# Performance work log

Hardware: AMD Instinct MI355X
Metric: run time of the kernel (lower is better)

The kernel has to match this reference:

```python
import jax, jax.numpy as jnp
import numpy as np

B, T, D = 8, 1024, 128
TEMP = 0.1
WEIGHT = 1.0


def _neg_scaled_l2(x, y):
    # x: [P, T, D], y: [P, S, D] -> -||x-y||^2 / D / TEMP  (l2 similarity, normalize_dimension=True)
    x2 = jnp.sum(x * x, axis=-1)[..., :, None]            # [P, T, 1]
    y2 = jnp.sum(y * y, axis=-1)[..., None, :]            # [P, 1, S]
    xy = jnp.einsum('ptd,psd->pts', x, y)                 # [P, T, S]
    d2 = jnp.maximum(x2 + y2 - 2.0 * xy, 0.0)             # cdist(...)**2 is non-negative
    return -d2 / D / TEMP


def setup_inputs() -> dict:
    key = jax.random.key(0)
    k1, k2, k3 = jax.random.split(key, 3)
    embs = jax.random.normal(k1, (B, T, D), dtype=jnp.float32)
    frame_idxs = jnp.sort(jax.random.randint(k2, (B, T), 0, 4096, dtype=jnp.int32), axis=-1)
    video_len = jax.random.randint(k3, (B,), T, 4096, dtype=jnp.int32)
    return {"embs": embs, "frame_idxs": frame_idxs, "video_len": video_len}


def reference(embs, frame_idxs, video_len):
    # All ordered pairs (i, j) with i != j, built at trace time.
    pairs = np.array([(i, j) for i in range(B) for j in range(B) if i != j])
    ii, jj = pairs[:, 0], pairs[:, 1]                     # [P]

    e1 = embs[ii]                                         # [P, T, D]
    e2 = embs[jj]                                         # [P, T, D]

    # Cycle: soft nearest neighbors of e1 in e2, then align back to e1.
    sim12 = _neg_scaled_l2(e1, e2)                        # [P, T, T]
    beta12 = jax.nn.softmax(sim12, axis=-1)
    nn_embs = jnp.einsum('pts,psd->ptd', beta12, e2)      # [P, T, D]
    logits = _neg_scaled_l2(nn_embs, e1)                  # [P, T, T]

    beta = jax.nn.softmax(logits, axis=-1)                # [P, T, T]
    steps = frame_idxs.astype(jnp.float32) / video_len.astype(jnp.float32)[:, None]  # [B, T]
    sp = steps[ii]                                        # [P, T] (steps of sequence i)
    time_true = sp                                        # one_hot(labels) picks the diagonal
    time_pred = jnp.einsum('pts,ps->pt', beta, sp)        # [P, T]
    loss = jnp.mean((time_pred - time_true) ** 2)
    return WEIGHT * loss
```

## Files before the change

### kernel.cpp

```cpp
#include <hip/hip_runtime.h>
#include <hip/hip_bf16.h>


#define T_ 1024
#define D_ 128
#define NPAIR 56
#define NSCALE 0.11271055006945026f
#define SQDS 0.474785316f

typedef float f32x16 __attribute__((ext_vector_type(16)));

#define B8F 131072
#define B8T 163840

__device__ __forceinline__ unsigned short f2bf(float f) {
  unsigned u = __float_as_uint(f);
  u += 0x7fff + ((u >> 16) & 1);
  return (unsigned short)(u >> 16);
}
__device__ __forceinline__ float bf2f(unsigned short v) {
  return __uint_as_float(((unsigned)v) << 16);
}
__device__ __forceinline__ float clamp8(float x) {
  return fminf(fmaxf(x, -440.f), 440.f);
}
__device__ __forceinline__ unsigned pk4(float a, float b, float c, float d) {
  int w = __builtin_amdgcn_cvt_pk_fp8_f32(a, b, 0, false);
  w = __builtin_amdgcn_cvt_pk_fp8_f32(c, d, w, true);
  return (unsigned)w;
}
__device__ __forceinline__ float waveSum(float v) {
#pragma unroll
  for (int k = 32; k >= 1; k >>= 1) v += __shfl_xor(v, k, 64);
  return v;
}
__device__ __forceinline__ void stage1k(const unsigned char* g, unsigned char* lds, int lane) {
  __builtin_amdgcn_global_load_lds(
      (const __attribute__((address_space(1))) unsigned int*)(g + lane * 16),
      (__attribute__((address_space(3))) unsigned int*)lds, 16, 0, 0);
}

__device__ __forceinline__ void c2b8(const unsigned* m, int lh, long long* b0, long long* b1) {
  unsigned send0 = lh ? m[0] : m[1];
  unsigned send1 = lh ? m[2] : m[3];
  unsigned r0 = (unsigned)__shfl_xor((int)send0, 32, 64);
  unsigned r1 = (unsigned)__shfl_xor((int)send1, 32, 64);
  union { unsigned u[2]; long long ll; } x0, x1;
  x0.u[0] = lh ? r0 : m[0];  x0.u[1] = lh ? m[1] : r0;
  x1.u[0] = lh ? r1 : m[2];  x1.u[1] = lh ? m[3] : r1;
  *b0 = x0.ll; *b1 = x1.ll;
}

#define MFMA8(A, B, C) __builtin_amdgcn_mfma_f32_32x32x16_fp8_fp8((A), (B), (C), 0, 0, 0)
#define LD8(P, Q) (*(const long long*)((P) + (Q) * 512))
#define EXPC(x) fminf(__builtin_amdgcn_exp2f(x), 448.f)
#define WAITV(N) asm volatile("s_waitcnt vmcnt(" #N ")" ::: "memory")
#define BAR() do { asm volatile("" ::: "memory"); __builtin_amdgcn_s_barrier(); asm volatile("" ::: "memory"); } while (0)

__global__ __launch_bounds__(256) void convert_kernel(
    const float* __restrict__ embs, const int* __restrict__ fi,
    const int* __restrict__ vl, unsigned char* __restrict__ e8F,
    unsigned char* __restrict__ e8T, float* __restrict__ steps,
    float* __restrict__ acc, unsigned* __restrict__ cnt) {
  __shared__ unsigned short tileS[32 * 136];
  __shared__ float psum[32][8];
  __shared__ float g_sh[32], sp_sh[32];
  const int b = blockIdx.x >> 5;
  const int t0 = (blockIdx.x & 31) * 32;
  const int tid = threadIdx.x;
  const int row = tid >> 3, seg = tid & 7;

  if (blockIdx.x == 0 && tid == 0) { acc[0] = 0.f; cnt[0] = 0u; }

  const float* src = embs + (size_t)(b * T_ + t0 + row) * D_ + seg * 16;
  float4 g4[4];
#pragma unroll
  for (int k = 0; k < 4; k++) g4[k] = ((const float4*)src)[k];
  float s = 0.f;
  float fv[16];
#pragma unroll
  for (int k = 0; k < 4; k++) {
    s += g4[k].x * g4[k].x + g4[k].y * g4[k].y + g4[k].z * g4[k].z + g4[k].w * g4[k].w;
    fv[4 * k + 0] = g4[k].x * SQDS; fv[4 * k + 1] = g4[k].y * SQDS;
    fv[4 * k + 2] = g4[k].z * SQDS; fv[4 * k + 3] = g4[k].w * SQDS;
  }
  psum[row][seg] = s;

  {
    unsigned char* dstA = e8F + (size_t)b * B8F + (size_t)((t0 >> 5) * 8 + seg) * 512;
    uint2 lo, hi;
    lo.x = pk4(fv[0], fv[1], fv[2], fv[3]);   lo.y = pk4(fv[4], fv[5], fv[6], fv[7]);
    hi.x = pk4(fv[8], fv[9], fv[10], fv[11]); hi.y = pk4(fv[12], fv[13], fv[14], fv[15]);
    *(uint2*)(dstA + row * 8) = lo;
    *(uint2*)(dstA + (size_t)(32 + row) * 8) = hi;
  }
#pragma unroll
  for (int k = 0; k < 16; k++) tileS[row * 136 + seg * 16 + k] = f2bf(fv[k]);
  __syncthreads();

  if (tid < 32) {
    float t = 0.f;
#pragma unroll
    for (int k = 0; k < 8; k++) t += psum[tid][k];
    int gr = b * T_ + t0 + tid;
    float sp = (float)fi[gr] / (float)vl[b];
    steps[gr] = sp;
    sp_sh[tid] = sp;
    g_sh[tid] = __builtin_amdgcn_exp2f(14.0f - t * NSCALE);
  }
  __syncthreads();

  {
    const int c8 = tid >> 5;
    const int n2 = c8 & 3, scp = c8 >> 2;
    const int dd = n2 * 32 + (tid & 31);
#pragma unroll
    for (int half = 0; half < 2; half++) {
      const int lane = half * 32 + (tid & 31);
      const int sl = scp * 16 + half * 8;
      float vv[8];
#pragma unroll
      for (int jj = 0; jj < 8; jj++)
        vv[jj] = clamp8(bf2f(tileS[(sl + jj) * 136 + dd]) * g_sh[sl + jj]);
      uint2 wv;
      wv.x = pk4(vv[0], vv[1], vv[2], vv[3]);
      wv.y = pk4(vv[4], vv[5], vv[6], vv[7]);
      int c = n2 * 64 + (t0 >> 4) + scp;
      *(uint2*)(e8T + (size_t)b * B8T + (size_t)c * 512 + lane * 8) = wv;
    }
  }
  if (tid < 128) {
    const int sc2 = tid >> 6, lane = tid & 63;
    const int m = lane & 31, kh = lane >> 5;
    uint2 wv; wv.x = 0u; wv.y = 0u;
    if (m < 2) {
      float vv[8];
#pragma unroll
      for (int e = 0; e < 8; e++) {
        int sl = sc2 * 16 + kh * 8 + e;
        float gg = g_sh[sl];
        vv[e] = clamp8(m ? gg * sp_sh[sl] : gg);
      }
      wv.x = pk4(vv[0], vv[1], vv[2], vv[3]);
      wv.y = pk4(vv[4], vv[5], vv[6], vv[7]);
    }
    int c = 256 + (t0 >> 4) + sc2;
    *(uint2*)(e8T + (size_t)b * B8T + (size_t)c * 512 + lane * 8) = wv;
  }
}

__global__ __launch_bounds__(256, 2) void tcc_main(
    const unsigned char* __restrict__ e8F, const unsigned char* __restrict__ e8T,
    const float* __restrict__ steps, float* __restrict__ loss_acc,
    unsigned* __restrict__ cnt, float* __restrict__ out) {
  __shared__ unsigned char smem[55296];
  __shared__ float blred[4];
  unsigned char* kt = smem;
  unsigned char* vt = smem + 24576;
  unsigned char* gt = smem + 24576;

  const int bx = blockIdx.x;
  const int pair = bx >> 3;
  const int tile = bx & 7;
  const int i = pair / 7;
  const int r = pair % 7;
  const int j = r + (r >= i ? 1 : 0);
  const int tid = threadIdx.x;
  const int w = tid >> 6;
  const int l = tid & 63;
  const int l31 = l & 31;
  const int lh = l >> 5;
  const int tb = tile * 128 + w * 32;

  const unsigned char* eFi = e8F + (size_t)i * B8F;
  const unsigned char* eFj = e8F + (size_t)j * B8F;
  const unsigned char* eTj = e8T + (size_t)j * B8T;
  const unsigned char* eTi = e8T + (size_t)i * B8T;

  long long qf8[8];
  {
    const unsigned char* qb = eFi + (size_t)((tb >> 5) * 8) * 512 + l * 8;
#pragma unroll
    for (int kc = 0; kc < 8; kc++) qf8[kc] = LD8(qb, kc);
  }

  const f32x16 Z = {0.f, 0.f, 0.f, 0.f, 0.f, 0.f, 0.f, 0.f,
                    0.f, 0.f, 0.f, 0.f, 0.f, 0.f, 0.f, 0.f};
  const f32x16 CM6 = {-6.f, -6.f, -6.f, -6.f, -6.f, -6.f, -6.f, -6.f,
                      -6.f, -6.f, -6.f, -6.f, -6.f, -6.f, -6.f, -6.f};
  f32x16 o[5];
#pragma unroll
  for (int n2 = 0; n2 < 5; n2++) o[n2] = Z;

  auto stageP1 = [&](int t, int b) {
    stage1k(eFj + (size_t)(8 * t + 2 * w) * 1024, kt + b * 8192 + (2 * w) * 1024, l);
    stage1k(eFj + (size_t)(8 * t + 2 * w + 1) * 1024, kt + b * 8192 + (2 * w + 1) * 1024, l);
#pragma unroll
    for (int u = 0; u < 3; u++) {
      int vu = w + 4 * u;
      if (vu < 10) {
        int n2v = vu >> 1, uh = vu & 1;
        stage1k(eTj + (size_t)(n2v * 32 + t * 2 + uh) * 1024, vt + b * 10240 + vu * 1024, l);
      }
    }
  };
  auto stageP2 = [&](int t, int b) {
    stage1k(eFi + (size_t)(8 * t + 2 * w) * 1024, kt + b * 8192 + (2 * w) * 1024, l);
    stage1k(eFi + (size_t)(8 * t + 2 * w + 1) * 1024, kt + b * 8192 + (2 * w + 1) * 1024, l);
    if (w < 2) stage1k(eTi + (size_t)(128 + t * 2 + w) * 1024, gt + b * 2048 + w * 1024, l);
  };

  stageP1(0, 0);
  stageP1(1, 1);
  WAITV(0);
  BAR();

  f32x16 ca0, ca1;
  {
    const unsigned char* kb = kt + l * 8;
    ca0 = MFMA8(LD8(kb, 0), qf8[0], CM6);
    ca1 = MFMA8(LD8(kb, 8), qf8[0], CM6);
#pragma unroll
    for (int dc = 1; dc < 8; dc++) {
      ca0 = MFMA8(LD8(kb, dc), qf8[dc], ca0);
      ca1 = MFMA8(LD8(kb, 8 + dc), qf8[dc], ca1);
    }
  }

  {
    int cur = 0, nxt = 1, pre = 2;
    for (int st = 0; st < 16; st++) {
      if (st <= 13) stageP1(st + 2, pre);
      __builtin_amdgcn_sched_barrier(0);

      f32x16 cb0, cb1;
      if (st < 15) {
        const unsigned char* kb = kt + nxt * 8192 + l * 8;
        cb0 = MFMA8(LD8(kb, 0), qf8[0], CM6);
        cb1 = MFMA8(LD8(kb, 8), qf8[0], CM6);
#pragma unroll
        for (int dc = 1; dc < 8; dc++) {
          cb0 = MFMA8(LD8(kb, dc), qf8[dc], cb0);
          cb1 = MFMA8(LD8(kb, 8 + dc), qf8[dc], cb1);
        }
      }

      unsigned m0[4], m1[4];
#pragma unroll
      for (int k2 = 0; k2 < 4; k2++) {
        m0[k2] = pk4(EXPC(ca0[4 * k2]), EXPC(ca0[4 * k2 + 1]),
                     EXPC(ca0[4 * k2 + 2]), EXPC(ca0[4 * k2 + 3]));
        m1[k2] = pk4(EXPC(ca1[4 * k2]), EXPC(ca1[4 * k2 + 1]),
                     EXPC(ca1[4 * k2 + 2]), EXPC(ca1[4 * k2 + 3]));
      }
      long long pB[4];
      c2b8(m0, lh, &pB[0], &pB[1]);
      c2b8(m1, lh, &pB[2], &pB[3]);

      const unsigned char* vb = vt + cur * 10240 + l * 8;
#pragma unroll
      for (int n2 = 0; n2 < 5; n2++)
#pragma unroll
        for (int sc = 0; sc < 4; sc++)
          o[n2] = MFMA8(LD8(vb, n2 * 4 + sc), pB[sc], o[n2]);

      if (st <= 13) {
        WAITV(0);
        BAR();
      } else if (st == 15) {
        BAR();
      }
      if (st < 15) { ca0 = cb0; ca1 = cb1; }
      int tswap = cur; cur = nxt; nxt = pre; pre = tswap;
    }
  }

  stageP2(0, 0);
  stageP2(1, 1);

  float Lme = o[4][0];
  float Lo = __shfl_xor(Lme, 32, 64);
  float inv = 1.0f / (lh ? Lo : Lme);
  long long qf2[8];
#pragma unroll
  for (int n2 = 0; n2 < 4; n2++) {
    unsigned mm[4];
#pragma unroll
    for (int k2 = 0; k2 < 4; k2++)
      mm[k2] = pk4(o[n2][4 * k2] * inv, o[n2][4 * k2 + 1] * inv,
                   o[n2][4 * k2 + 2] * inv, o[n2][4 * k2 + 3] * inv);
    c2b8(mm, lh, &qf2[2 * n2], &qf2[2 * n2 + 1]);
  }
  f32x16 acc6 = Z;
  WAITV(0);
  BAR();

  f32x16 da0, da1;
  {
    const unsigned char* kb = kt + l * 8;
    da0 = MFMA8(LD8(kb, 0), qf2[0], CM6);
    da1 = MFMA8(LD8(kb, 8), qf2[0], CM6);
#pragma unroll
    for (int dc = 1; dc < 8; dc++) {
      da0 = MFMA8(LD8(kb, dc), qf2[dc], da0);
      da1 = MFMA8(LD8(kb, 8 + dc), qf2[dc], da1);
    }
  }

  {
    int cur = 0, nxt = 1, pre = 2;
    for (int st = 0; st < 16; st++) {
      if (st <= 13) stageP2(st + 2, pre);
      __builtin_amdgcn_sched_barrier(0);

      f32x16 db0, db1;
      if (st < 15) {
        const unsigned char* kb = kt + nxt * 8192 + l * 8;
        db0 = MFMA8(LD8(kb, 0), qf2[0], CM6);
        db1 = MFMA8(LD8(kb, 8), qf2[0], CM6);
#pragma unroll
        for (int dc = 1; dc < 8; dc++) {
          db0 = MFMA8(LD8(kb, dc), qf2[dc], db0);
          db1 = MFMA8(LD8(kb, 8 + dc), qf2[dc], db1);
        }
      }

      unsigned m0[4], m1[4];
#pragma unroll
      for (int k2 = 0; k2 < 4; k2++) {
        m0[k2] = pk4(EXPC(da0[4 * k2]), EXPC(da0[4 * k2 + 1]),
                     EXPC(da0[4 * k2 + 2]), EXPC(da0[4 * k2 + 3]));
        m1[k2] = pk4(EXPC(da1[4 * k2]), EXPC(da1[4 * k2 + 1]),
                     EXPC(da1[4 * k2 + 2]), EXPC(da1[4 * k2 + 3]));
      }
      long long pB[4];
      c2b8(m0, lh, &pB[0], &pB[1]);
      c2b8(m1, lh, &pB[2], &pB[3]);

      const unsigned char* gb = gt + cur * 2048 + l * 8;
#pragma unroll
      for (int sc = 0; sc < 4; sc++)
        acc6 = MFMA8(LD8(gb, sc), pB[sc], acc6);

      if (st <= 13) {
        WAITV(0);
        BAR();
      }
      if (st < 15) { da0 = db0; da1 = db1; }
      int tswap = cur; cur = nxt; nxt = pre; pre = tswap;
    }
  }

  float local = 0.f;
  if (lh == 0) {
    float pred = acc6[1] / acc6[0];
    float tt = steps[i * T_ + tb + l31];
    float dd = pred - tt;
    local = dd * dd;
  }
  local = waveSum(local);
  if (l == 0) blred[w] = local;
  __syncthreads();
  if (tid == 0) {
    atomicAdd(loss_acc, blred[0] + blred[1] + blred[2] + blred[3]);
    __threadfence();
    unsigned old = atomicAdd(cnt, 1u);
    if (old == (unsigned)(gridDim.x - 1)) {
      float v = atomicAdd(loss_acc, 0.0f);
      out[0] = v * (1.0f / (float)(NPAIR * T_));
    }
  }
}

extern "C" void kernel_launch(void* const* d_in, const int* in_sizes, int n_in,
                              void* d_out, int out_size, void* d_ws, size_t ws_size,
                              hipStream_t stream) {
  const float* embs = (const float*)d_in[0];
  const int* frame_idxs = (const int*)d_in[1];
  const int* video_len = (const int*)d_in[2];
  float* out = (float*)d_out;

  char* ws = (char*)d_ws;
  float* acc = (float*)ws;
  unsigned* cnt = (unsigned*)(ws + 512);
  float* steps = (float*)(ws + 4096);
  unsigned char* e8F = (unsigned char*)(ws + 65536);
  unsigned char* e8T = e8F + (size_t)8 * B8F;

  convert_kernel<<<dim3(256), dim3(256), 0, stream>>>(embs, frame_idxs, video_len,
                                                      e8F, e8T, steps, acc, cnt);
  tcc_main<<<dim3(NPAIR * 8), dim3(256), 0, stream>>>(e8F, e8T, steps, acc, cnt, out);
}
```

Measured before the change: 114.4 us.

## Fuse conversion kernel into main kernel with a global spin-wait barrier

```diff
diff --git a/kernel.cpp b/kernel.cpp
--- a/kernel.cpp
+++ b/kernel.cpp
@@ -57,102 +57,12 @@
 #define WAITV(N) asm volatile("s_waitcnt vmcnt(" #N ")" ::: "memory")
 #define BAR() do { asm volatile("" ::: "memory"); __builtin_amdgcn_s_barrier(); asm volatile("" ::: "memory"); } while (0)
 
-__global__ __launch_bounds__(256) void convert_kernel(
+__global__ __launch_bounds__(256, 2) void fused_main(
     const float* __restrict__ embs, const int* __restrict__ fi,
     const int* __restrict__ vl, unsigned char* __restrict__ e8F,
     unsigned char* __restrict__ e8T, float* __restrict__ steps,
-    float* __restrict__ acc, unsigned* __restrict__ cnt) {
-  __shared__ unsigned short tileS[32 * 136];
-  __shared__ float psum[32][8];
-  __shared__ float g_sh[32], sp_sh[32];
-  const int b = blockIdx.x >> 5;
-  const int t0 = (blockIdx.x & 31) * 32;
-  const int tid = threadIdx.x;
-  const int row = tid >> 3, seg = tid & 7;
-
-  if (blockIdx.x == 0 && tid == 0) { acc[0] = 0.f; cnt[0] = 0u; }
-
-  const float* src = embs + (size_t)(b * T_ + t0 + row) * D_ + seg * 16;
-  float4 g4[4];
-#pragma unroll
-  for (int k = 0; k < 4; k++) g4[k] = ((const float4*)src)[k];
-  float s = 0.f;
-  float fv[16];
-#pragma unroll
-  for (int k = 0; k < 4; k++) {
-    s += g4[k].x * g4[k].x + g4[k].y * g4[k].y + g4[k].z * g4[k].z + g4[k].w * g4[k].w;
-    fv[4 * k + 0] = g4[k].x * SQDS; fv[4 * k + 1] = g4[k].y * SQDS;
-    fv[4 * k + 2] = g4[k].z * SQDS; fv[4 * k + 3] = g4[k].w * SQDS;
-  }
-  psum[row][seg] = s;
-
-  {
-    unsigned char* dstA = e8F + (size_t)b * B8F + (size_t)((t0 >> 5) * 8 + seg) * 512;
-    uint2 lo, hi;
-    lo.x = pk4(fv[0], fv[1], fv[2], fv[3]);   lo.y = pk4(fv[4], fv[5], fv[6], fv[7]);
-    hi.x = pk4(fv[8], fv[9], fv[10], fv[11]); hi.y = pk4(fv[12], fv[13], fv[14], fv[15]);
-    *(uint2*)(dstA + row * 8) = lo;
-    *(uint2*)(dstA + (size_t)(32 + row) * 8) = hi;
-  }
-#pragma unroll
-  for (int k = 0; k < 16; k++) tileS[row * 136 + seg * 16 + k] = f2bf(fv[k]);
-  __syncthreads();
-
-  if (tid < 32) {
-    float t = 0.f;
-#pragma unroll
-    for (int k = 0; k < 8; k++) t += psum[tid][k];
-    int gr = b * T_ + t0 + tid;
-    float sp = (float)fi[gr] / (float)vl[b];
-    steps[gr] = sp;
-    sp_sh[tid] = sp;
-    g_sh[tid] = __builtin_amdgcn_exp2f(14.0f - t * NSCALE);
-  }
-  __syncthreads();
-
-  {
-    const int c8 = tid >> 5;
-    const int n2 = c8 & 3, scp = c8 >> 2;
-    const int dd = n2 * 32 + (tid & 31);
-#pragma unroll
-    for (int half = 0; half < 2; half++) {
-      const int lane = half * 32 + (tid & 31);
-      const int sl = scp * 16 + half * 8;
-      float vv[8];
-#pragma unroll
-      for (int jj = 0; jj < 8; jj++)
-        vv[jj] = clamp8(bf2f(tileS[(sl + jj) * 136 + dd]) * g_sh[sl + jj]);
-      uint2 wv;
-      wv.x = pk4(vv[0], vv[1], vv[2], vv[3]);
-      wv.y = pk4(vv[4], vv[5], vv[6], vv[7]);
-      int c = n2 * 64 + (t0 >> 4) + scp;
-      *(uint2*)(e8T + (size_t)b * B8T + (size_t)c * 512 + lane * 8) = wv;
-    }
-  }
-  if (tid < 128) {
-    const int sc2 = tid >> 6, lane = tid & 63;
-    const int m = lane & 31, kh = lane >> 5;
-    uint2 wv; wv.x = 0u; wv.y = 0u;
-    if (m < 2) {
-      float vv[8];
-#pragma unroll
-      for (int e = 0; e < 8; e++) {
-        int sl = sc2 * 16 + kh * 8 + e;
-        float gg = g_sh[sl];
-        vv[e] = clamp8(m ? gg * sp_sh[sl] : gg);
-      }
-      wv.x = pk4(vv[0], vv[1], vv[2], vv[3]);
-      wv.y = pk4(vv[4], vv[5], vv[6], vv[7]);
-    }
-    int c = 256 + (t0 >> 4) + sc2;
-    *(uint2*)(e8T + (size_t)b * B8T + (size_t)c * 512 + lane * 8) = wv;
-  }
-}
-
-__global__ __launch_bounds__(256, 2) void tcc_main(
-    const unsigned char* __restrict__ e8F, const unsigned char* __restrict__ e8T,
-    const float* __restrict__ steps, float* __restrict__ loss_acc,
-    unsigned* __restrict__ cnt, float* __restrict__ out) {
+    float* __restrict__ loss_acc, unsigned* __restrict__ cnt,
+    unsigned* __restrict__ cvt, float* __restrict__ out) {
   __shared__ unsigned char smem[55296];
   __shared__ float blred[4];
   unsigned char* kt = smem;
@@ -160,12 +70,108 @@
   unsigned char* gt = smem + 24576;
 
   const int bx = blockIdx.x;
+  const int tid = threadIdx.x;
+
+  if (bx < 256) {
+    unsigned short* tileS = (unsigned short*)smem;
+    float* psum = (float*)(smem + 8704);
+    float* g_sh = (float*)(smem + 9728);
+    float* sp_sh = (float*)(smem + 9856);
+    const int b = bx >> 5;
+    const int t0 = (bx & 31) * 32;
+    const int row = tid >> 3, seg = tid & 7;
+
+    const float* src = embs + (size_t)(b * T_ + t0 + row) * D_ + seg * 16;
+    float4 g4[4];
+#pragma unroll
+    for (int k = 0; k < 4; k++) g4[k] = ((const float4*)src)[k];
+    float s = 0.f;
+    float fv[16];
+#pragma unroll
+    for (int k = 0; k < 4; k++) {
+      s += g4[k].x * g4[k].x + g4[k].y * g4[k].y + g4[k].z * g4[k].z + g4[k].w * g4[k].w;
+      fv[4 * k + 0] = g4[k].x * SQDS; fv[4 * k + 1] = g4[k].y * SQDS;
+      fv[4 * k + 2] = g4[k].z * SQDS; fv[4 * k + 3] = g4[k].w * SQDS;
+    }
+    psum[row * 8 + seg] = s;
+
+    {
+      unsigned char* dstA = e8F + (size_t)b * B8F + (size_t)((t0 >> 5) * 8 + seg) * 512;
+      uint2 lo, hi;
+      lo.x = pk4(fv[0], fv[1], fv[2], fv[3]);   lo.y = pk4(fv[4], fv[5], fv[6], fv[7]);
+      hi.x = pk4(fv[8], fv[9], fv[10], fv[11]); hi.y = pk4(fv[12], fv[13], fv[14], fv[15]);
+      *(uint2*)(dstA + row * 8) = lo;
+      *(uint2*)(dstA + (size_t)(32 + row) * 8) = hi;
+    }
+#pragma unroll
+    for (int k = 0; k < 16; k++) tileS[row * 136 + seg * 16 + k] = f2bf(fv[k]);
+    __syncthreads();
+
+    if (tid < 32) {
+      float t = 0.f;
+#pragma unroll
+      for (int k = 0; k < 8; k++) t += psum[tid * 8 + k];
+      int gr = b * T_ + t0 + tid;
+      float sp = (float)fi[gr] / (float)vl[b];
+      steps[gr] = sp;
+      sp_sh[tid] = sp;
+      g_sh[tid] = __builtin_amdgcn_exp2f(14.0f - t * NSCALE);
+    }
+    __syncthreads();
+
+    {
+      const int c8 = tid >> 5;
+      const int n2 = c8 & 3, scp = c8 >> 2;
+      const int dd = n2 * 32 + (tid & 31);
+#pragma unroll
+      for (int half = 0; half < 2; half++) {
+        const int lane = half * 32 + (tid & 31);
+        const int sl = scp * 16 + half * 8;
+        float vv[8];
+#pragma unroll
+        for (int jj = 0; jj < 8; jj++)
+          vv[jj] = clamp8(bf2f(tileS[(sl + jj) * 136 + dd]) * g_sh[sl + jj]);
+        uint2 wv;
+        wv.x = pk4(vv[0], vv[1], vv[2], vv[3]);
+        wv.y = pk4(vv[4], vv[5], vv[6], vv[7]);
+        int c = n2 * 64 + (t0 >> 4) + scp;
+        *(uint2*)(e8T + (size_t)b * B8T + (size_t)c * 512 + lane * 8) = wv;
+      }
+    }
+    if (tid < 128) {
+      const int sc2 = tid >> 6, lane = tid & 63;
+      const int m = lane & 31, kh = lane >> 5;
+      uint2 wv; wv.x = 0u; wv.y = 0u;
+      if (m < 2) {
+        float vv[8];
+#pragma unroll
+        for (int e = 0; e < 8; e++) {
+          int sl = sc2 * 16 + kh * 8 + e;
+          float gg = g_sh[sl];
+          vv[e] = clamp8(m ? gg * sp_sh[sl] : gg);
+        }
+        wv.x = pk4(vv[0], vv[1], vv[2], vv[3]);
+        wv.y = pk4(vv[4], vv[5], vv[6], vv[7]);
+      }
+      int c = 256 + (t0 >> 4) + sc2;
+      *(uint2*)(e8T + (size_t)b * B8T + (size_t)c * 512 + lane * 8) = wv;
+    }
+    __syncthreads();
+    __threadfence();
+    if (tid == 0) atomicAdd(cvt, 1u);
+  }
+
+  if (tid == 0) {
+    while (atomicAdd(cvt, 0u) < 256u) __builtin_amdgcn_s_sleep(2);
+  }
+  __syncthreads();
+  __threadfence();
+
   const int pair = bx >> 3;
   const int tile = bx & 7;
   const int i = pair / 7;
   const int r = pair % 7;
   const int j = r + (r >= i ? 1 : 0);
-  const int tid = threadIdx.x;
   const int w = tid >> 6;
   const int l = tid & 63;
   const int l31 = l & 31;
@@ -383,11 +389,13 @@
   char* ws = (char*)d_ws;
   float* acc = (float*)ws;
   unsigned* cnt = (unsigned*)(ws + 512);
+  unsigned* cvt = (unsigned*)(ws + 1024);
   float* steps = (float*)(ws + 4096);
   unsigned char* e8F = (unsigned char*)(ws + 65536);
   unsigned char* e8T = e8F + (size_t)8 * B8F;
 
-  convert_kernel<<<dim3(256), dim3(256), 0, stream>>>(embs, frame_idxs, video_len,
-                                                      e8F, e8T, steps, acc, cnt);
-  tcc_main<<<dim3(NPAIR * 8), dim3(256), 0, stream>>>(e8F, e8T, steps, acc, cnt, out);
-}
+  hipMemsetAsync(ws, 0, 2048, stream);
+
+  fused_main<<<dim3(NPAIR * 8), dim3(256), 0, stream>>>(
+      embs, frame_idxs, video_len, e8F, e8T, steps, acc, cnt, cvt, out);
+}
```

Measured after the change: 174.9 us. +52.8%, slower.
